# Kernel optimization log

Hardware: AMD Instinct MI355X
Metric: run time of the kernel (lower is better)

Reference implementation:

```python
import jax, jax.numpy as jnp
import numpy as np

HIDDEN = 1024
HEADS = 16
HEAD_DIM = HIDDEN // HEADS


def setup_inputs() -> dict:
    key = jax.random.key(0)
    k1, k2, k3, k4, k5 = jax.random.split(key, 5)
    B, S = 2, 2048
    x = jax.random.normal(k1, (B, S, HIDDEN), dtype=jnp.float32)
    attention_mask = jnp.ones((B, S), dtype=jnp.int32)
    scale = 1.0 / np.sqrt(HIDDEN)
    W_qkv = jax.random.normal(k2, (HIDDEN, 3 * HIDDEN), dtype=jnp.float32) * scale
    b_qkv = jnp.zeros((3 * HIDDEN,), dtype=jnp.float32)
    W_out = jax.random.normal(k3, (HIDDEN, HIDDEN), dtype=jnp.float32) * scale
    b_out = jnp.zeros((HIDDEN,), dtype=jnp.float32)
    return {"x": x, "attention_mask": attention_mask, "W_qkv": W_qkv,
            "b_qkv": b_qkv, "W_out": W_out, "b_out": b_out}


def reference(x, attention_mask, W_qkv, b_qkv, W_out, b_out):
    B, S, H = x.shape
    qkv = x @ W_qkv + b_qkv                       # [B,S,3H]
    q, k, v = jnp.split(qkv, 3, axis=-1)
    def heads(t):
        return t.reshape(B, S, HEADS, HEAD_DIM).transpose(0, 2, 1, 3)  # [B,h,S,d]
    q, k, v = heads(q), heads(k), heads(v)
    scale = 1.0 / np.sqrt(HEAD_DIM).astype(np.float32)
    scores = jnp.einsum('bhsd,bhtd->bhst', q, k) * scale  # [B,h,S,S]
    causal = jnp.triu(jnp.full((S, S), -jnp.inf, dtype=scores.dtype), k=1)
    scores = scores + causal
    pad = (attention_mask == 0)[:, None, None, :]          # [B,1,1,S]
    scores = jnp.where(pad, -jnp.inf, scores)
    probs = jax.nn.softmax(scores, axis=-1)
    context = jnp.einsum('bhst,bhtd->bhsd', probs, v)
    context = context.transpose(0, 2, 1, 3).reshape(B, S, H)
    output = context @ W_out + b_out
    return (output, q, k, v)
```

## Files before the change

kernel.cpp:

```cpp
#include <hip/hip_runtime.h>
#include <hip/hip_bf16.h>
#include <stdint.h>

typedef __attribute__((ext_vector_type(8))) short bf16x8;
typedef __attribute__((ext_vector_type(4))) float f32x4;

#define GLD16(gp, lp) __builtin_amdgcn_global_load_lds( \
    (const __attribute__((address_space(1))) void*)(gp), \
    (__attribute__((address_space(3))) void*)(lp), 16, 0, 0)

struct bf16_4 { __hip_bfloat16 x, y, z, w; };

__global__ __launch_bounds__(256) void k_conv(const float* __restrict__ in,
                                              __hip_bfloat16* __restrict__ out, int n4)
{
    int i = blockIdx.x * 256 + threadIdx.x;
    if (i >= n4) return;
    float4 v = ((const float4*)in)[i];
    bf16_4 o = { __float2bfloat16(v.x), __float2bfloat16(v.y),
                 __float2bfloat16(v.z), __float2bfloat16(v.w) };
    ((bf16_4*)out)[i] = o;
}

__global__ __launch_bounds__(256) void k_tconv(const float* __restrict__ in,
                                               __hip_bfloat16* __restrict__ out,
                                               int R, int C)
{
    __shared__ float tile[32][33];
    int c0 = blockIdx.x * 32, r0 = blockIdx.y * 32;
    int tc = threadIdx.x & 31, tr = threadIdx.x >> 5;
#pragma unroll
    for (int i = 0; i < 4; i++)
        tile[tr + i * 8][tc] = in[(size_t)(r0 + tr + i * 8) * C + c0 + tc];
    __syncthreads();
#pragma unroll
    for (int i = 0; i < 4; i++) {
        int r = tr + i * 8;
        out[(size_t)(c0 + r) * R + r0 + tc] = __float2bfloat16(tile[tc][r]);
    }
}

__global__ __launch_bounds__(256) void k_vtrans(const __hip_bfloat16* __restrict__ vin,
                                                __hip_bfloat16* __restrict__ vout)
{
    __shared__ __hip_bfloat16 t[64 * 80];
    const int kt = blockIdx.x, bh = blockIdx.y;
    const int tid = threadIdx.x;
    const size_t ib = (size_t)bh * 131072;
#pragma unroll
    for (int i = 0; i < 2; i++) {
        int c = i * 256 + tid;
        int kv = c >> 3, d0 = (c & 7) * 8;
        bf16x8 vv = *(const bf16x8*)(vin + ib + (size_t)(kt * 64 + kv) * 64 + d0);
#pragma unroll
        for (int j = 0; j < 8; j++)
            t[(d0 + j) * 80 + kv] = ((const __hip_bfloat16*)&vv)[j];
    }
    __syncthreads();
#pragma unroll
    for (int i = 0; i < 2; i++) {
        int c = i * 256 + tid;
        int d = c >> 3, kv0 = (c & 7) * 8;
        *(bf16x8*)(vout + ib + (size_t)d * 2048 + kt * 64 + kv0) =
            *(const bf16x8*)(t + d * 80 + kv0);
    }
}

template <int EPI>
__global__ __launch_bounds__(256) void k_gemm(const __hip_bfloat16* __restrict__ A,
                                              const __hip_bfloat16* __restrict__ Bt,
                                              const float* __restrict__ bias,
                                              float* __restrict__ outf,
                                              __hip_bfloat16* __restrict__ outb,
                                              int M, int N, int K)
{
    __shared__ __hip_bfloat16 As[128 * 32];
    __shared__ __hip_bfloat16 Bs[128 * 32];

    const int tid  = threadIdx.x;
    const int lane = tid & 63, wid = tid >> 6;
    const int wrow = wid >> 1, wcol = wid & 1;
    const int lr = lane & 15, lg = lane >> 4;
    const int m0 = blockIdx.y * 128, n0 = blockIdx.x * 128;

    f32x4 acc[4][4] = {};

    for (int k0 = 0; k0 < K; k0 += 32) {
        __syncthreads();
#pragma unroll
        for (int i = 0; i < 2; i++) {
            int c = i * 256 + tid;
            const __hip_bfloat16* ga = A + (size_t)(m0 + (c >> 2)) * K + k0 + (c & 3) * 8;
            GLD16(ga, As + (size_t)(i * 256 + wid * 64) * 8);
            const __hip_bfloat16* gb = Bt + (size_t)(n0 + (c >> 2)) * K + k0 + (c & 3) * 8;
            GLD16(gb, Bs + (size_t)(i * 256 + wid * 64) * 8);
        }
        __syncthreads();

        bf16x8 af[4], bfr[4];
#pragma unroll
        for (int mi = 0; mi < 4; mi++)
            af[mi] = *(const bf16x8*)(As + (wrow * 64 + mi * 16 + lr) * 32 + 8 * lg);
#pragma unroll
        for (int ni = 0; ni < 4; ni++)
            bfr[ni] = *(const bf16x8*)(Bs + (wcol * 64 + ni * 16 + lr) * 32 + 8 * lg);
#pragma unroll
        for (int mi = 0; mi < 4; mi++)
#pragma unroll
            for (int ni = 0; ni < 4; ni++)
                acc[mi][ni] = __builtin_amdgcn_mfma_f32_16x16x32_bf16(af[mi], bfr[ni], acc[mi][ni], 0, 0, 0);
    }

#pragma unroll
    for (int mi = 0; mi < 4; mi++) {
#pragma unroll
        for (int ni = 0; ni < 4; ni++) {
#pragma unroll
            for (int j = 0; j < 4; j++) {
                int mg = m0 + wrow * 64 + mi * 16 + 4 * lg + j;
                int ng = n0 + wcol * 64 + ni * 16 + lr;
                float val = acc[mi][ni][j] + bias[ng];
                if (EPI == 0) {
                    int part = ng >> 10;
                    int h    = (ng >> 6) & 15;
                    int dd   = ng & 63;
                    int b    = mg >> 11;
                    int s    = mg & 2047;
                    size_t idx = ((size_t)part << 22) + ((((size_t)b * 16 + h) * 2048 + s) << 6) + dd;
                    outf[idx] = val;
                    outb[idx] = __float2bfloat16(val);
                } else {
                    outf[(size_t)mg * N + ng] = val;
                }
            }
        }
    }
}

__global__ __launch_bounds__(256, 3) void k_attn2(const __hip_bfloat16* __restrict__ qkv,
                                                  const __hip_bfloat16* __restrict__ vT,
                                                  const int* __restrict__ amask,
                                                  __hip_bfloat16* __restrict__ ctx)
{
    const int bx = blockIdx.x;
    const int bh = blockIdx.y;
    const int b = bh >> 4, h = bh & 15;
    const int tid = threadIdx.x;
    const int lane = tid & 63, w = tid >> 6;
    const int lr = lane & 15, lg = lane >> 4;
    const size_t hb = (size_t)bh * (2048 * 64);
    const __hip_bfloat16* qg = qkv + hb;
    const __hip_bfloat16* kg = qkv + ((size_t)1 << 22) + hb;
    const __hip_bfloat16* vt = vT + (size_t)bh * (64 * 2048);

    __shared__ __hip_bfloat16 Ks[128 * 64];
    __shared__ __hip_bfloat16 Vs[64 * 128];
    __shared__ __hip_bfloat16 Ps[4][16 * 128];
    __shared__ float maskadd[128];

#pragma unroll 1
    for (int pass = 0; pass < 2; ++pass) {
        const int qt = pass ? bx : (31 - bx);
        const int q0 = qt * 64;
        const int nkt = (64 * qt + 191) >> 7;

        bf16x8 qf[2];
#pragma unroll
        for (int kk = 0; kk < 2; kk++)
            qf[kk] = *(const bf16x8*)(qg + (size_t)(q0 + w * 16 + lr) * 64 + kk * 32 + 8 * lg);

        f32x4 of[4] = {};
        float m_run[4], l_run[4];
#pragma unroll
        for (int j = 0; j < 4; j++) { m_run[j] = -1e30f; l_run[j] = 0.f; }
        const int rowg = q0 + w * 16 + 4 * lg;

#pragma unroll 1
        for (int kt = 0; kt < nkt; ++kt) {
            const int k0 = kt * 128;
            __syncthreads();
#pragma unroll
            for (int i = 0; i < 4; i++) {
                int c = i * 256 + tid;
                int r = c >> 3, sl = c & 7;
                GLD16(kg + (size_t)(k0 + r) * 64 + ((sl ^ (r & 7)) * 8),
                      Ks + (size_t)(i * 256 + w * 64) * 8);
            }
#pragma unroll
            for (int i = 0; i < 4; i++) {
                int c = i * 256 + tid;
                int r = c >> 4, sl = c & 15;
                GLD16(vt + (size_t)r * 2048 + k0 + ((sl ^ (r & 15)) * 8),
                      Vs + (size_t)(i * 256 + w * 64) * 8);
            }
            if (tid < 128) maskadd[tid] = amask[b * 2048 + k0 + tid] ? 0.f : -1e30f;
            __syncthreads();

            f32x4 sa[8] = {};
#pragma unroll
            for (int ni = 0; ni < 8; ni++) {
                int r = ni * 16 + lr;
#pragma unroll
                for (int kk = 0; kk < 2; kk++) {
                    bf16x8 kf = *(const bf16x8*)(Ks + (size_t)r * 64 + (((kk * 4 + lg) ^ (r & 7)) * 8));
                    sa[ni] = __builtin_amdgcn_mfma_f32_16x16x32_bf16(qf[kk], kf, sa[ni], 0, 0, 0);
                }
            }
#pragma unroll
            for (int ni = 0; ni < 8; ni++) {
                int colg = k0 + ni * 16 + lr;
                float ma = maskadd[ni * 16 + lr];
#pragma unroll
                for (int j = 0; j < 4; j++) {
                    float val = sa[ni][j] * 0.125f + ma;
                    if (colg > rowg + j) val = -1e30f;
                    sa[ni][j] = val;
                }
            }
            float mnew[4], corr[4];
#pragma unroll
            for (int j = 0; j < 4; j++) {
                float t = fmaxf(fmaxf(fmaxf(sa[0][j], sa[1][j]), fmaxf(sa[2][j], sa[3][j])),
                                fmaxf(fmaxf(sa[4][j], sa[5][j]), fmaxf(sa[6][j], sa[7][j])));
                t = fmaxf(t, __shfl_xor(t, 1));
                t = fmaxf(t, __shfl_xor(t, 2));
                t = fmaxf(t, __shfl_xor(t, 4));
                t = fmaxf(t, __shfl_xor(t, 8));
                mnew[j] = fmaxf(m_run[j], t);
                corr[j] = __expf(m_run[j] - mnew[j]);
                m_run[j] = mnew[j];
            }
            float tsum[4] = {0.f, 0.f, 0.f, 0.f};
#pragma unroll
            for (int ni = 0; ni < 8; ni++)
#pragma unroll
                for (int j = 0; j < 4; j++) {
                    float p = __expf(sa[ni][j] - mnew[j]);
                    sa[ni][j] = p;
                    tsum[j] += p;
                }
#pragma unroll
            for (int j = 0; j < 4; j++) {
                float t = tsum[j];
                t += __shfl_xor(t, 1);
                t += __shfl_xor(t, 2);
                t += __shfl_xor(t, 4);
                t += __shfl_xor(t, 8);
                l_run[j] = l_run[j] * corr[j] + t;
#pragma unroll
                for (int nd = 0; nd < 4; nd++) of[nd][j] *= corr[j];
            }
#pragma unroll
            for (int ni = 0; ni < 8; ni++)
#pragma unroll
                for (int j = 0; j < 4; j++) {
                    int row = 4 * lg + j, col = ni * 16 + lr;
                    Ps[w][row * 128 + (((col >> 3) ^ row) * 8) + (col & 7)] =
                        __float2bfloat16(sa[ni][j]);
                }
            asm volatile("s_waitcnt lgkmcnt(0)" ::: "memory");
            __builtin_amdgcn_sched_barrier(0);
#pragma unroll
            for (int kk = 0; kk < 4; kk++) {
                bf16x8 pf = *(const bf16x8*)(&Ps[w][lr * 128 + (((kk * 4 + lg) ^ lr) * 8)]);
#pragma unroll
                for (int nd = 0; nd < 4; nd++) {
                    int r = nd * 16 + lr;
                    bf16x8 vf = *(const bf16x8*)(Vs + (size_t)r * 128 + (((kk * 4 + lg) ^ (r & 15)) * 8));
                    of[nd] = __builtin_amdgcn_mfma_f32_16x16x32_bf16(pf, vf, of[nd], 0, 0, 0);
                }
            }
        }
#pragma unroll
        for (int j = 0; j < 4; j++) {
            float inv = 1.f / l_run[j];
            int s = rowg + j;
            size_t base = ((size_t)b * 2048 + s) * 1024 + h * 64;
#pragma unroll
            for (int nd = 0; nd < 4; nd++)
                ctx[base + nd * 16 + lr] = __float2bfloat16(of[nd][j] * inv);
        }
    }
}

extern "C" void kernel_launch(void* const* d_in, const int* in_sizes, int n_in,
                              void* d_out, int out_size, void* d_ws, size_t ws_size,
                              hipStream_t stream)
{
    const float* x    = (const float*)d_in[0];
    const int*   am   = (const int*)d_in[1];
    const float* Wqkv = (const float*)d_in[2];
    const float* bqkv = (const float*)d_in[3];
    const float* Wout = (const float*)d_in[4];
    const float* bout = (const float*)d_in[5];
    float* out = (float*)d_out;

    char* ws = (char*)d_ws;
    __hip_bfloat16* x_bf   = (__hip_bfloat16*)(ws);
    __hip_bfloat16* Wqkv_t = (__hip_bfloat16*)(ws + ((size_t)8 << 20));
    __hip_bfloat16* Wout_t = (__hip_bfloat16*)(ws + ((size_t)14 << 20));
    __hip_bfloat16* qkv_bf = (__hip_bfloat16*)(ws + ((size_t)16 << 20));
    __hip_bfloat16* ctx_bf = (__hip_bfloat16*)(ws + ((size_t)40 << 20));
    __hip_bfloat16* vT     = x_bf;

    k_conv<<<4096, 256, 0, stream>>>(x, x_bf, 1048576);
    k_tconv<<<dim3(96, 32), 256, 0, stream>>>(Wqkv, Wqkv_t, 1024, 3072);
    k_tconv<<<dim3(32, 32), 256, 0, stream>>>(Wout, Wout_t, 1024, 1024);
    k_gemm<0><<<dim3(24, 32), 256, 0, stream>>>(x_bf, Wqkv_t, bqkv,
                                                out + ((size_t)1 << 22), qkv_bf,
                                                4096, 3072, 1024);
    k_vtrans<<<dim3(32, 32), 256, 0, stream>>>(qkv_bf + ((size_t)2 << 22), vT);
    k_attn2<<<dim3(16, 32), 256, 0, stream>>>(qkv_bf, vT, am, ctx_bf);
    k_gemm<1><<<dim3(8, 32), 256, 0, stream>>>(ctx_bf, Wout_t, bout,
                                               out, nullptr,
                                               4096, 1024, 1024);
}
```

Measured before the change: 251.8 us.

## Rewrite GEMMs with double-buffered LDS, XOR swizzle, K=64 tiles and larger QKV tile

Replaces the single-buffered GEMM with a templated kernel that double-buffers LDS, so the async global-to-LDS loads for the next K tile overlap the MFMA work on the current one. K tiles grow from 32 to 64, and an XOR swizzle is applied to LDS rows to avoid bank conflicts. The QKV projection now uses 256x192 tiles with 512 threads, and s_setprio is raised around the MFMA section. The cost is more LDS per block (about 112KB for the QKV config), which may limit occupancy, and the QKV grid shrinks to 256 blocks.

```diff
diff --git a/kernel.cpp b/kernel.cpp
--- a/kernel.cpp
+++ b/kernel.cpp
@@ -66,59 +66,89 @@
     }
 }
 
-template <int EPI>
-__global__ __launch_bounds__(256) void k_gemm(const __hip_bfloat16* __restrict__ A,
-                                              const __hip_bfloat16* __restrict__ Bt,
-                                              const float* __restrict__ bias,
-                                              float* __restrict__ outf,
-                                              __hip_bfloat16* __restrict__ outb,
-                                              int M, int N, int K)
-{
-    __shared__ __hip_bfloat16 As[128 * 32];
-    __shared__ __hip_bfloat16 Bs[128 * 32];
+template <int BM, int BN, int TM, int TN, int EPI>
+__global__ __launch_bounds__(TM * TN * 64, 2) void k_gemm2(
+    const __hip_bfloat16* __restrict__ A,
+    const __hip_bfloat16* __restrict__ Bt,
+    const float* __restrict__ bias,
+    float* __restrict__ outf,
+    __hip_bfloat16* __restrict__ outb,
+    int M, int N, int K)
+{
+    constexpr int THREADS = TM * TN * 64;
+    constexpr int NMI = BM / TM / 16;
+    constexpr int NNI = BN / TN / 16;
+    constexpr int ACH = BM * 8 / THREADS;
+    constexpr int BCH = BN * 8 / THREADS;
+
+    __shared__ __hip_bfloat16 As[2][BM * 64];
+    __shared__ __hip_bfloat16 Bs[2][BN * 64];
 
     const int tid  = threadIdx.x;
     const int lane = tid & 63, wid = tid >> 6;
-    const int wrow = wid >> 1, wcol = wid & 1;
+    const int wm = wid / TN, wn = wid % TN;
     const int lr = lane & 15, lg = lane >> 4;
-    const int m0 = blockIdx.y * 128, n0 = blockIdx.x * 128;
-
-    f32x4 acc[4][4] = {};
-
-    for (int k0 = 0; k0 < K; k0 += 32) {
+    const int m0 = blockIdx.y * BM, n0 = blockIdx.x * BN;
+    const int NT = K >> 6;
+
+    f32x4 acc[NMI][NNI] = {};
+
+    auto stage = [&](int bb, int t) {
+#pragma unroll
+        for (int i = 0; i < ACH; i++) {
+            int c = i * THREADS + tid;
+            int r = c >> 3, sl = c & 7;
+            GLD16(A + (size_t)(m0 + r) * K + t * 64 + ((sl ^ (r & 7)) * 8),
+                  &As[bb][(size_t)(i * THREADS + wid * 64) * 8]);
+        }
+#pragma unroll
+        for (int i = 0; i < BCH; i++) {
+            int c = i * THREADS + tid;
+            int r = c >> 3, sl = c & 7;
+            GLD16(Bt + (size_t)(n0 + r) * K + t * 64 + ((sl ^ (r & 7)) * 8),
+                  &Bs[bb][(size_t)(i * THREADS + wid * 64) * 8]);
+        }
+    };
+
+    stage(0, 0);
+    __syncthreads();
+    int cur = 0;
+#pragma unroll 1
+    for (int t = 0; t < NT; ++t) {
+        if (t + 1 < NT) stage(cur ^ 1, t + 1);
+        __builtin_amdgcn_s_setprio(1);
+        bf16x8 bfr[NNI][2];
+#pragma unroll
+        for (int ni = 0; ni < NNI; ni++) {
+            int r = wn * (BN / TN) + ni * 16 + lr;
+#pragma unroll
+            for (int kk = 0; kk < 2; kk++)
+                bfr[ni][kk] = *(const bf16x8*)(&Bs[cur][r * 64 + (((kk * 4 + lg) ^ (r & 7)) * 8)]);
+        }
+#pragma unroll
+        for (int mi = 0; mi < NMI; mi++) {
+            int r = wm * (BM / TM) + mi * 16 + lr;
+            bf16x8 a0 = *(const bf16x8*)(&As[cur][r * 64 + (((0 + lg) ^ (r & 7)) * 8)]);
+            bf16x8 a1 = *(const bf16x8*)(&As[cur][r * 64 + (((4 + lg) ^ (r & 7)) * 8)]);
+#pragma unroll
+            for (int ni = 0; ni < NNI; ni++) {
+                acc[mi][ni] = __builtin_amdgcn_mfma_f32_16x16x32_bf16(a0, bfr[ni][0], acc[mi][ni], 0, 0, 0);
+                acc[mi][ni] = __builtin_amdgcn_mfma_f32_16x16x32_bf16(a1, bfr[ni][1], acc[mi][ni], 0, 0, 0);
+            }
+        }
+        __builtin_amdgcn_s_setprio(0);
         __syncthreads();
-#pragma unroll
-        for (int i = 0; i < 2; i++) {
-            int c = i * 256 + tid;
-            const __hip_bfloat16* ga = A + (size_t)(m0 + (c >> 2)) * K + k0 + (c & 3) * 8;
-            GLD16(ga, As + (size_t)(i * 256 + wid * 64) * 8);
-            const __hip_bfloat16* gb = Bt + (size_t)(n0 + (c >> 2)) * K + k0 + (c & 3) * 8;
-            GLD16(gb, Bs + (size_t)(i * 256 + wid * 64) * 8);
-        }
-        __syncthreads();
-
-        bf16x8 af[4], bfr[4];
-#pragma unroll
-        for (int mi = 0; mi < 4; mi++)
-            af[mi] = *(const bf16x8*)(As + (wrow * 64 + mi * 16 + lr) * 32 + 8 * lg);
-#pragma unroll
-        for (int ni = 0; ni < 4; ni++)
-            bfr[ni] = *(const bf16x8*)(Bs + (wcol * 64 + ni * 16 + lr) * 32 + 8 * lg);
-#pragma unroll
-        for (int mi = 0; mi < 4; mi++)
-#pragma unroll
-            for (int ni = 0; ni < 4; ni++)
-                acc[mi][ni] = __builtin_amdgcn_mfma_f32_16x16x32_bf16(af[mi], bfr[ni], acc[mi][ni], 0, 0, 0);
-    }
-
-#pragma unroll
-    for (int mi = 0; mi < 4; mi++) {
-#pragma unroll
-        for (int ni = 0; ni < 4; ni++) {
+        cur ^= 1;
+    }
+
+#pragma unroll
+    for (int mi = 0; mi < NMI; mi++) {
+#pragma unroll
+        for (int ni = 0; ni < NNI; ni++) {
 #pragma unroll
             for (int j = 0; j < 4; j++) {
-                int mg = m0 + wrow * 64 + mi * 16 + 4 * lg + j;
-                int ng = n0 + wcol * 64 + ni * 16 + lr;
+                int mg = m0 + wm * (BM / TM) + mi * 16 + 4 * lg + j;
+                int ng = n0 + wn * (BN / TN) + ni * 16 + lr;
                 float val = acc[mi][ni][j] + bias[ng];
                 if (EPI == 0) {
                     int part = ng >> 10;
@@ -306,12 +336,10 @@
     k_conv<<<4096, 256, 0, stream>>>(x, x_bf, 1048576);
     k_tconv<<<dim3(96, 32), 256, 0, stream>>>(Wqkv, Wqkv_t, 1024, 3072);
     k_tconv<<<dim3(32, 32), 256, 0, stream>>>(Wout, Wout_t, 1024, 1024);
-    k_gemm<0><<<dim3(24, 32), 256, 0, stream>>>(x_bf, Wqkv_t, bqkv,
-                                                out + ((size_t)1 << 22), qkv_bf,
-                                                4096, 3072, 1024);
+    k_gemm2<256, 192, 2, 4, 0><<<dim3(16, 16), 512, 0, stream>>>(
+        x_bf, Wqkv_t, bqkv, out + ((size_t)1 << 22), qkv_bf, 4096, 3072, 1024);
     k_vtrans<<<dim3(32, 32), 256, 0, stream>>>(qkv_bf + ((size_t)2 << 22), vT);
     k_attn2<<<dim3(16, 32), 256, 0, stream>>>(qkv_bf, vT, am, ctx_bf);
-    k_gemm<1><<<dim3(8, 32), 256, 0, stream>>>(ctx_bf, Wout_t, bout,
-                                               out, nullptr,
-                                               4096, 1024, 1024);
-}
+    k_gemm2<128, 128, 2, 2, 1><<<dim3(8, 32), 256, 0, stream>>>(
+        ctx_bf, Wout_t, bout, out, nullptr, 4096, 1024, 1024);
+}
```

Measured after the change: 231.6 us. -8.0%, faster.
